# Performance work log

Hardware: AMD Instinct MI355X
Metric: run time of the kernel (lower is better)

## Reference

```python
import jax, jax.numpy as jnp
import numpy as np

# Dimensions per init_kwargs
B, S, D = 2, 2048, 1024          # batch, seq, hidden_size
F = 4096                          # intermediate_size
E, K = 8, 2                       # moe_num_experts, moe_top_k
EPS = 1e-9


def setup_inputs() -> dict:
    key = jax.random.key(0)
    k1, k2, k3, k4 = jax.random.split(key, 4)
    x = jax.random.normal(k1, (B, S, D), dtype=jnp.float32)
    # gate: Linear(D, E, bias=False) -> stored as [D, E] for x @ w_gate
    w_gate = jax.random.normal(k2, (D, E), dtype=jnp.float32) * 0.02
    # per-expert gate_up_proj: Linear(D, 2F, bias=False), stacked over experts -> [E, D, 2F]
    w_gate_up = jax.random.normal(k3, (E, D, 2 * F), dtype=jnp.float32) * 0.02
    # per-expert down_proj: Linear(F, D, bias=False), stacked -> [E, F, D]
    w_down = jax.random.normal(k4, (E, F, D), dtype=jnp.float32) * 0.02
    return {"x": x, "w_gate": w_gate, "w_gate_up": w_gate_up, "w_down": w_down}


def reference(x, w_gate, w_gate_up, w_down):
    # Router
    gate_logits = x @ w_gate                       # [B,S,E]
    gate_probs = jax.nn.softmax(gate_logits, axis=-1)
    # top-k masking + renormalization (top_k < num_experts)
    topk_vals, topk_idx = jax.lax.top_k(gate_probs, K)           # [B,S,K]
    masked = jnp.sum(jax.nn.one_hot(topk_idx, E, dtype=gate_probs.dtype)
                     * topk_vals[..., None], axis=-2)            # [B,S,E]
    denom = jnp.maximum(jnp.sum(masked, axis=-1, keepdims=True), EPS)
    gate_probs = masked / denom

    # Dense per-expert SwiGLU FFN on all tokens (faithful to reference impl)
    gu = jnp.einsum('bsd,edh->ebsh', x, w_gate_up)               # [E,B,S,2F]
    g, u = jnp.split(gu, 2, axis=-1)                             # [E,B,S,F] each
    act = jax.nn.silu(g) * u                                     # [E,B,S,F]
    expert_out = jnp.einsum('ebsf,efd->ebsd', act, w_down)       # [E,B,S,D]

    # Gate-weighted combine
    return jnp.einsum('bse,ebsd->bsd', gate_probs, expert_out)   # [B,S,D]
```

## Files before the change

kernel.cpp:

```cpp
#include <hip/hip_runtime.h>
#include <stdint.h>

#define NTOK 4096
#define DMODEL 1024
#define FF 4096
#define NEXP 8

typedef __bf16 bf16x8 __attribute__((ext_vector_type(8)));
typedef float f32x4 __attribute__((ext_vector_type(4)));
typedef unsigned short u16x8 __attribute__((ext_vector_type(8)));

__device__ __forceinline__ unsigned short f2bf(float f) {
  union { float f; unsigned u; } v; v.f = f;
  unsigned r = v.u + 0x7fffu + ((v.u >> 16) & 1u);
  return (unsigned short)(r >> 16);
}

__global__ __launch_bounds__(256) void k_convert_x(const float4* __restrict__ in,
                                                   ushort4* __restrict__ out, int n4) {
  int stride = gridDim.x * blockDim.x;
  for (int i = blockIdx.x * blockDim.x + threadIdx.x; i < n4; i += stride) {
    float4 v = in[i];
    out[i] = make_ushort4(f2bf(v.x), f2bf(v.y), f2bf(v.z), f2bf(v.w));
  }
}

__global__ __launch_bounds__(256) void k_transpose_bf16(const float* __restrict__ in,
                                                        unsigned short* __restrict__ out,
                                                        int R, int C) {
  __shared__ float tile[64][65];
  const size_t slab = (size_t)R * C;
  const float* ip = in + slab * blockIdx.z;
  unsigned short* op = out + slab * blockIdx.z;
  int c0 = blockIdx.x * 64, r0 = blockIdx.y * 64;
  int tx = threadIdx.x & 15, ty = threadIdx.x >> 4;
#pragma unroll
  for (int i = 0; i < 4; ++i) {
    int r = ty + 16 * i;
    float4 v = *(const float4*)(ip + (size_t)(r0 + r) * C + c0 + tx * 4);
    tile[r][tx * 4 + 0] = v.x;
    tile[r][tx * 4 + 1] = v.y;
    tile[r][tx * 4 + 2] = v.z;
    tile[r][tx * 4 + 3] = v.w;
  }
  __syncthreads();
  int w = threadIdx.x >> 6, lane = threadIdx.x & 63;
  int rc = (lane & 7) * 8;
#pragma unroll
  for (int pass = 0; pass < 2; ++pass) {
    int c = pass * 32 + w * 8 + (lane >> 3);
    u16x8 o;
#pragma unroll
    for (int j = 0; j < 8; ++j) o[j] = f2bf(tile[rc + j][c]);
    *(u16x8*)(op + (size_t)(c0 + c) * R + r0 + rc) = o;
  }
}

__global__ __launch_bounds__(256) void k_router(const float* __restrict__ x,
                                                const float* __restrict__ wg,
                                                int* __restrict__ cnt,
                                                int* __restrict__ elist,
                                                float* __restrict__ gw) {
  int wave = threadIdx.x >> 6, lane = threadIdx.x & 63;
  int t = blockIdx.x * 4 + wave;
  const float* xp = x + (size_t)t * DMODEL;
  float a[8] = {0, 0, 0, 0, 0, 0, 0, 0};
#pragma unroll
  for (int i = 0; i < DMODEL / 64; ++i) {
    int d = lane + 64 * i;
    float xv = xp[d];
    float4 w0 = *(const float4*)(wg + d * 8);
    float4 w1 = *(const float4*)(wg + d * 8 + 4);
    a[0] += xv * w0.x; a[1] += xv * w0.y; a[2] += xv * w0.z; a[3] += xv * w0.w;
    a[4] += xv * w1.x; a[5] += xv * w1.y; a[6] += xv * w1.z; a[7] += xv * w1.w;
  }
#pragma unroll
  for (int off = 32; off > 0; off >>= 1)
#pragma unroll
    for (int e = 0; e < 8; ++e) a[e] += __shfl_down(a[e], off, 64);
  if (lane == 0) {
    int e0 = 0;
    for (int e = 1; e < 8; ++e) if (a[e] > a[e0]) e0 = e;
    int e1 = (e0 == 0) ? 1 : 0;
    for (int e = 0; e < 8; ++e) if (e != e0 && a[e] > a[e1]) e1 = e;
    float p = __expf(a[e1] - a[e0]);
    float inv = 1.0f / (1.0f + p);
    int p0 = atomicAdd(&cnt[e0], 1);
    elist[e0 * NTOK + p0] = 2 * t;
    gw[2 * t] = inv;
    int p1 = atomicAdd(&cnt[e1], 1);
    elist[e1 * NTOK + p1] = 2 * t + 1;
    gw[2 * t + 1] = p * inv;
  }
}

__global__ __launch_bounds__(512, 4) void k_gemm1(const unsigned short* __restrict__ xb,
                                                  const unsigned short* __restrict__ wgu,
                                                  const int* __restrict__ cnt,
                                                  const int* __restrict__ elist,
                                                  unsigned short* __restrict__ act)
{
  __shared__ __align__(16) unsigned short sA[2][128 * 64];
  __shared__ __align__(16) unsigned short sB[2][128 * 64];

  const int e = blockIdx.z;
  const int n_e = cnt[e];
  const int m0 = blockIdx.y * 128;
  if (m0 >= n_e) return;
  const int c0 = blockIdx.x * 64;
  int abase = 0;
#pragma unroll
  for (int j = 0; j < NEXP; ++j) abase += (j < e) ? cnt[j] : 0;
  const int tid = threadIdx.x;
  const int w = tid >> 6, lane = tid & 63;
  const int wr = w >> 2, wc = w & 3;
  const int* el = elist + e * NTOK;
  const int csub = ((lane & 7) ^ (lane >> 3)) * 8;
  const int srow = w * 8 + (lane >> 3);

  int tokrow[2];
  size_t baddr[2];
  const unsigned short* wb = wgu + (size_t)e * (2 * FF) * DMODEL;
#pragma unroll
  for (int i = 0; i < 2; ++i) {
    int r = i * 64 + srow;
    int idx = m0 + r;
    tokrow[i] = el[idx < n_e ? idx : 0] >> 1;
    int strip = r >> 5, off = r & 31;
    int wrow = (off < 16) ? (c0 + strip * 16 + off) : (FF + c0 + strip * 16 + off - 16);
    baddr[i] = (size_t)wrow * DMODEL;
  }

  f32x4 acc[4][2];
  f32x4 zero = {0.f, 0.f, 0.f, 0.f};
#pragma unroll
  for (int m = 0; m < 4; ++m)
#pragma unroll
    for (int n = 0; n < 2; ++n) acc[m][n] = zero;

  auto stage = [&](int buf, int k0) {
#pragma unroll
    for (int i = 0; i < 2; ++i) {
      const unsigned short* g2 = xb + (size_t)tokrow[i] * DMODEL + k0 + csub;
      __builtin_amdgcn_global_load_lds((const __attribute__((address_space(1))) void*)g2,
                                       (__attribute__((address_space(3))) void*)(&sA[buf][(i * 64 + w * 8) * 64]),
                                       16, 0, 0);
    }
#pragma unroll
    for (int i = 0; i < 2; ++i) {
      const unsigned short* g2 = wb + baddr[i] + k0 + csub;
      __builtin_amdgcn_global_load_lds((const __attribute__((address_space(1))) void*)g2,
                                       (__attribute__((address_space(3))) void*)(&sB[buf][(i * 64 + w * 8) * 64]),
                                       16, 0, 0);
    }
  };

  auto compute = [&](int buf) {
#pragma unroll
    for (int kk = 0; kk < 2; ++kk) {
      const int xk = ((kk * 4 + (lane >> 4)) ^ (lane & 7)) * 8;
      bf16x8 af[4], bf[2];
#pragma unroll
      for (int m = 0; m < 4; ++m)
        af[m] = *(const bf16x8*)(&sA[buf][(wr * 64 + m * 16 + (lane & 15)) * 64 + xk]);
#pragma unroll
      for (int n = 0; n < 2; ++n)
        bf[n] = *(const bf16x8*)(&sB[buf][(wc * 32 + n * 16 + (lane & 15)) * 64 + xk]);
#pragma unroll
      for (int m = 0; m < 4; ++m)
#pragma unroll
        for (int n = 0; n < 2; ++n)
          acc[m][n] = __builtin_amdgcn_mfma_f32_16x16x32_bf16(af[m], bf[n], acc[m][n], 0, 0, 0);
    }
  };

  stage(0, 0);
  __syncthreads();
  int cur = 0;
  for (int t = 0; t < DMODEL / 64; ++t) {
    if (t + 1 < DMODEL / 64) stage(cur ^ 1, (t + 1) * 64);
    compute(cur);
    __syncthreads();
    cur ^= 1;
  }

#pragma unroll
  for (int m = 0; m < 4; ++m) {
#pragma unroll
    for (int r = 0; r < 4; ++r) {
      int idx = m0 + wr * 64 + m * 16 + (lane >> 4) * 4 + r;
      if (idx < n_e) {
        unsigned short* ap = act + (size_t)(abase + idx) * FF + c0 + wc * 16;
        float gv = acc[m][0][r];
        float u = acc[m][1][r];
        float s = gv / (1.0f + __expf(-gv));
        ap[lane & 15] = f2bf(s * u);
      }
    }
  }
}

__global__ __launch_bounds__(256, 4) void k_gemm2(const unsigned short* __restrict__ actb,
                                                  const unsigned short* __restrict__ wd,
                                                  const int* __restrict__ cnt,
                                                  const int* __restrict__ elist,
                                                  const float* __restrict__ gw,
                                                  float* __restrict__ out)
{
  __shared__ __align__(16) unsigned short sA[128 * 64];
  __shared__ __align__(16) unsigned short sB[128 * 64];

  const int bid = blockIdx.x;
  const int e = bid & 7;
  const int within = bid >> 3;
  const int kc = within >> 8;
  const int y = (within >> 3) & 31;
  const int xcol = within & 7;
  const int n_e = cnt[e];
  const int m0 = y * 128;
  if (m0 >= n_e) return;
  const int n0 = xcol * 128;
  int abase = 0;
#pragma unroll
  for (int j = 0; j < NEXP; ++j) abase += (j < e) ? cnt[j] : 0;
  const int tid = threadIdx.x;
  const int w = tid >> 6, lane = tid & 63;
  const int wr = w >> 1, wc = w & 1;
  const int* el = elist + e * NTOK;
  const int csub = ((lane & 7) ^ (lane >> 3)) * 8;

  int arow[4];
  size_t baddr[4];
  const unsigned short* wb = wd + (size_t)e * DMODEL * FF;
#pragma unroll
  for (int i = 0; i < 4; ++i) {
    int r = i * 32 + w * 8 + (lane >> 3);
    int idx = m0 + r;
    arow[i] = abase + (idx < n_e ? idx : 0);
    baddr[i] = (size_t)(n0 + r) * FF;
  }

  f32x4 acc[4][4];
  f32x4 zero = {0.f, 0.f, 0.f, 0.f};
#pragma unroll
  for (int m = 0; m < 4; ++m)
#pragma unroll
    for (int n = 0; n < 4; ++n) acc[m][n] = zero;

  const int kbeg = kc * 1024, kend = kbeg + 1024;
  for (int k0 = kbeg; k0 < kend; k0 += 64) {
#pragma unroll
    for (int i = 0; i < 4; ++i) {
      const unsigned short* g2 = actb + (size_t)arow[i] * FF + k0 + csub;
      __builtin_amdgcn_global_load_lds((const __attribute__((address_space(1))) void*)g2,
                                       (__attribute__((address_space(3))) void*)(&sA[(i * 32 + w * 8) * 64]),
                                       16, 0, 0);
    }
#pragma unroll
    for (int i = 0; i < 4; ++i) {
      const unsigned short* g2 = wb + baddr[i] + k0 + csub;
      __builtin_amdgcn_global_load_lds((const __attribute__((address_space(1))) void*)g2,
                                       (__attribute__((address_space(3))) void*)(&sB[(i * 32 + w * 8) * 64]),
                                       16, 0, 0);
    }
    __syncthreads();
#pragma unroll
    for (int kk = 0; kk < 2; ++kk) {
      const int xk = ((kk * 4 + (lane >> 4)) ^ (lane & 7)) * 8;
      bf16x8 af[4], bf[4];
#pragma unroll
      for (int m = 0; m < 4; ++m)
        af[m] = *(const bf16x8*)(&sA[(wr * 64 + m * 16 + (lane & 15)) * 64 + xk]);
#pragma unroll
      for (int n = 0; n < 4; ++n)
        bf[n] = *(const bf16x8*)(&sB[(wc * 64 + n * 16 + (lane & 15)) * 64 + xk]);
#pragma unroll
      for (int m = 0; m < 4; ++m)
#pragma unroll
        for (int n = 0; n < 4; ++n)
          acc[m][n] = __builtin_amdgcn_mfma_f32_16x16x32_bf16(af[m], bf[n], acc[m][n], 0, 0, 0);
    }
    __syncthreads();
  }

#pragma unroll
  for (int m = 0; m < 4; ++m) {
#pragma unroll
    for (int r = 0; r < 4; ++r) {
      int idx = m0 + wr * 64 + m * 16 + (lane >> 4) * 4 + r;
      if (idx < n_e) {
        int p = el[idx];
        float wgt = gw[p];
        float* op = out + (size_t)(p >> 1) * DMODEL + n0 + wc * 64;
#pragma unroll
        for (int n = 0; n < 4; ++n)
          atomicAdd(&op[n * 16 + (lane & 15)], acc[m][n][r] * wgt);
      }
    }
  }
}

extern "C" void kernel_launch(void* const* d_in, const int* in_sizes, int n_in,
                              void* d_out, int out_size, void* d_ws, size_t ws_size,
                              hipStream_t stream) {
  const float* x   = (const float*)d_in[0];
  const float* wg  = (const float*)d_in[1];
  const float* wgu = (const float*)d_in[2];
  const float* wd  = (const float*)d_in[3];
  float* out = (float*)d_out;

  char* ws = (char*)d_ws;
  size_t off = 0;
  auto alloc = [&](size_t bytes) -> char* {
    char* p = ws + off;
    off += (bytes + 255) & ~(size_t)255;
    return p;
  };
  unsigned short* wgu_t = (unsigned short*)alloc((size_t)NEXP * 2 * FF * DMODEL * 2);
  unsigned short* wd_t  = (unsigned short*)alloc((size_t)NEXP * DMODEL * FF * 2);
  unsigned short* actb  = (unsigned short*)alloc((size_t)2 * NTOK * FF * 2);
  unsigned short* xb    = (unsigned short*)alloc((size_t)NTOK * DMODEL * 2);
  int* elist            = (int*)alloc((size_t)NEXP * NTOK * 4);
  float* gw             = (float*)alloc((size_t)2 * NTOK * 4);
  int* cnt              = (int*)alloc(256);
  if (off > ws_size) return;

  hipMemsetAsync(cnt, 0, 256, stream);
  hipMemsetAsync(out, 0, (size_t)NTOK * DMODEL * 4, stream);
  k_convert_x<<<1024, 256, 0, stream>>>((const float4*)x, (ushort4*)xb, NTOK * DMODEL / 4);
  k_transpose_bf16<<<dim3(2 * FF / 64, DMODEL / 64, NEXP), 256, 0, stream>>>(wgu, wgu_t, DMODEL, 2 * FF);
  k_transpose_bf16<<<dim3(DMODEL / 64, FF / 64, NEXP), 256, 0, stream>>>(wd, wd_t, FF, DMODEL);
  k_router<<<NTOK / 4, 256, 0, stream>>>(x, wg, cnt, elist, gw);
  k_gemm1<<<dim3(FF / 64, NTOK / 128, NEXP), 512, 0, stream>>>(xb, wgu_t, cnt, elist, actb);
  k_gemm2<<<8192, 256, 0, stream>>>(actb, wd_t, cnt, elist, gw, out);
}
```

Measured before the change: 582.2 us.

## Double-buffer gemm2 LDS tiles and remove split-K atomics

Rewrites the down-projection GEMM to process the full K dimension per block instead of four split-K chunks, and double-buffers the A/B LDS tiles so the next tile's global-to-LDS loads overlap the current MFMA work. Blocks grow to 512 threads with each wave computing a 64x32 sub-tile. This cuts the atomic adds to the output by a factor of four and hides load latency, but reduces the number of blocks and doubles LDS usage, which may lower occupancy and parallelism.

```diff
diff --git a/kernel.cpp b/kernel.cpp
--- a/kernel.cpp
+++ b/kernel.cpp
@@ -200,21 +200,20 @@
   }
 }
 
-__global__ __launch_bounds__(256, 4) void k_gemm2(const unsigned short* __restrict__ actb,
+__global__ __launch_bounds__(512, 4) void k_gemm2(const unsigned short* __restrict__ actb,
                                                   const unsigned short* __restrict__ wd,
                                                   const int* __restrict__ cnt,
                                                   const int* __restrict__ elist,
                                                   const float* __restrict__ gw,
                                                   float* __restrict__ out)
 {
-  __shared__ __align__(16) unsigned short sA[128 * 64];
-  __shared__ __align__(16) unsigned short sB[128 * 64];
+  __shared__ __align__(16) unsigned short sA[2][128 * 64];
+  __shared__ __align__(16) unsigned short sB[2][128 * 64];
 
   const int bid = blockIdx.x;
   const int e = bid & 7;
   const int within = bid >> 3;
-  const int kc = within >> 8;
-  const int y = (within >> 3) & 31;
+  const int y = within >> 3;
   const int xcol = within & 7;
   const int n_e = cnt[e];
   const int m0 = y * 128;
@@ -225,62 +224,72 @@
   for (int j = 0; j < NEXP; ++j) abase += (j < e) ? cnt[j] : 0;
   const int tid = threadIdx.x;
   const int w = tid >> 6, lane = tid & 63;
-  const int wr = w >> 1, wc = w & 1;
+  const int wr = w >> 2, wc = w & 3;
   const int* el = elist + e * NTOK;
   const int csub = ((lane & 7) ^ (lane >> 3)) * 8;
-
-  int arow[4];
-  size_t baddr[4];
+  const int srow = w * 8 + (lane >> 3);
+
+  int arow[2];
+  size_t baddr[2];
   const unsigned short* wb = wd + (size_t)e * DMODEL * FF;
 #pragma unroll
-  for (int i = 0; i < 4; ++i) {
-    int r = i * 32 + w * 8 + (lane >> 3);
-    int idx = m0 + r;
+  for (int i = 0; i < 2; ++i) {
+    int idx = m0 + i * 64 + srow;
     arow[i] = abase + (idx < n_e ? idx : 0);
-    baddr[i] = (size_t)(n0 + r) * FF;
-  }
-
-  f32x4 acc[4][4];
+    baddr[i] = (size_t)(n0 + i * 64 + srow) * FF;
+  }
+
+  f32x4 acc[4][2];
   f32x4 zero = {0.f, 0.f, 0.f, 0.f};
 #pragma unroll
   for (int m = 0; m < 4; ++m)
 #pragma unroll
-    for (int n = 0; n < 4; ++n) acc[m][n] = zero;
-
-  const int kbeg = kc * 1024, kend = kbeg + 1024;
-  for (int k0 = kbeg; k0 < kend; k0 += 64) {
-#pragma unroll
-    for (int i = 0; i < 4; ++i) {
+    for (int n = 0; n < 2; ++n) acc[m][n] = zero;
+
+  auto stage = [&](int buf, int k0) {
+#pragma unroll
+    for (int i = 0; i < 2; ++i) {
       const unsigned short* g2 = actb + (size_t)arow[i] * FF + k0 + csub;
       __builtin_amdgcn_global_load_lds((const __attribute__((address_space(1))) void*)g2,
-                                       (__attribute__((address_space(3))) void*)(&sA[(i * 32 + w * 8) * 64]),
+                                       (__attribute__((address_space(3))) void*)(&sA[buf][(i * 64 + w * 8) * 64]),
                                        16, 0, 0);
     }
 #pragma unroll
-    for (int i = 0; i < 4; ++i) {
+    for (int i = 0; i < 2; ++i) {
       const unsigned short* g2 = wb + baddr[i] + k0 + csub;
       __builtin_amdgcn_global_load_lds((const __attribute__((address_space(1))) void*)g2,
-                                       (__attribute__((address_space(3))) void*)(&sB[(i * 32 + w * 8) * 64]),
+                                       (__attribute__((address_space(3))) void*)(&sB[buf][(i * 64 + w * 8) * 64]),
                                        16, 0, 0);
     }
-    __syncthreads();
+  };
+
+  auto compute = [&](int buf) {
 #pragma unroll
     for (int kk = 0; kk < 2; ++kk) {
       const int xk = ((kk * 4 + (lane >> 4)) ^ (lane & 7)) * 8;
-      bf16x8 af[4], bf[4];
+      bf16x8 af[4], bf[2];
 #pragma unroll
       for (int m = 0; m < 4; ++m)
-        af[m] = *(const bf16x8*)(&sA[(wr * 64 + m * 16 + (lane & 15)) * 64 + xk]);
-#pragma unroll
-      for (int n = 0; n < 4; ++n)
-        bf[n] = *(const bf16x8*)(&sB[(wc * 64 + n * 16 + (lane & 15)) * 64 + xk]);
+        af[m] = *(const bf16x8*)(&sA[buf][(wr * 64 + m * 16 + (lane & 15)) * 64 + xk]);
+#pragma unroll
+      for (int n = 0; n < 2; ++n)
+        bf[n] = *(const bf16x8*)(&sB[buf][(wc * 32 + n * 16 + (lane & 15)) * 64 + xk]);
 #pragma unroll
       for (int m = 0; m < 4; ++m)
 #pragma unroll
-        for (int n = 0; n < 4; ++n)
+        for (int n = 0; n < 2; ++n)
           acc[m][n] = __builtin_amdgcn_mfma_f32_16x16x32_bf16(af[m], bf[n], acc[m][n], 0, 0, 0);
     }
+  };
+
+  stage(0, 0);
+  __syncthreads();
+  int cur = 0;
+  for (int t = 0; t < FF / 64; ++t) {
+    if (t + 1 < FF / 64) stage(cur ^ 1, (t + 1) * 64);
+    compute(cur);
     __syncthreads();
+    cur ^= 1;
   }
 
 #pragma unroll
@@ -291,9 +300,9 @@
       if (idx < n_e) {
         int p = el[idx];
         float wgt = gw[p];
-        float* op = out + (size_t)(p >> 1) * DMODEL + n0 + wc * 64;
-#pragma unroll
-        for (int n = 0; n < 4; ++n)
+        float* op = out + (size_t)(p >> 1) * DMODEL + n0 + wc * 32;
+#pragma unroll
+        for (int n = 0; n < 2; ++n)
           atomicAdd(&op[n * 16 + (lane & 15)], acc[m][n][r] * wgt);
       }
     }
@@ -332,5 +341,5 @@
   k_transpose_bf16<<<dim3(DMODEL / 64, FF / 64, NEXP), 256, 0, stream>>>(wd, wd_t, FF, DMODEL);
   k_router<<<NTOK / 4, 256, 0, stream>>>(x, wg, cnt, elist, gw);
   k_gemm1<<<dim3(FF / 64, NTOK / 128, NEXP), 512, 0, stream>>>(xb, wgu_t, cnt, elist, actb);
-  k_gemm2<<<8192, 256, 0, stream>>>(actb, wd_t, cnt, elist, gw, out);
-}
+  k_gemm2<<<2048, 512, 0, stream>>>(actb, wd_t, cnt, elist, gw, out);
+}
```

New measurement: 588.0 us. No clear change (+1.0%).

## Replace split-K atomics in down-proj with per-slot stores and combine kernel

Applied to the files above, without the earlier changes.

The down-projection GEMM no longer splits K four ways with float atomicAdd into the output. Each block now runs the full FF reduction and writes a weighted result to a per-(token, slot) buffer, and a new combine kernel sums the two slots per token. Activations are stored indexed by slot id instead of by a compacted expert offset, and the block-to-tile mapping is changed. This removes atomic traffic and the output memset, at the cost of an extra 32MB buffer pass, 4x fewer gemm2 blocks (lower parallelism) and scattered activation rows.

```diff
diff --git a/kernel.cpp b/kernel.cpp
--- a/kernel.cpp
+++ b/kernel.cpp
@@ -108,9 +108,6 @@
   const int m0 = blockIdx.y * 128;
   if (m0 >= n_e) return;
   const int c0 = blockIdx.x * 64;
-  int abase = 0;
-#pragma unroll
-  for (int j = 0; j < NEXP; ++j) abase += (j < e) ? cnt[j] : 0;
   const int tid = threadIdx.x;
   const int w = tid >> 6, lane = tid & 63;
   const int wr = w >> 2, wc = w & 3;
@@ -190,7 +187,8 @@
     for (int r = 0; r < 4; ++r) {
       int idx = m0 + wr * 64 + m * 16 + (lane >> 4) * 4 + r;
       if (idx < n_e) {
-        unsigned short* ap = act + (size_t)(abase + idx) * FF + c0 + wc * 16;
+        int p = el[idx];
+        unsigned short* ap = act + (size_t)p * FF + c0 + wc * 16;
         float gv = acc[m][0][r];
         float u = acc[m][1][r];
         float s = gv / (1.0f + __expf(-gv));
@@ -205,38 +203,34 @@
                                                   const int* __restrict__ cnt,
                                                   const int* __restrict__ elist,
                                                   const float* __restrict__ gw,
-                                                  float* __restrict__ out)
+                                                  float* __restrict__ out_slot)
 {
   __shared__ __align__(16) unsigned short sA[128 * 64];
   __shared__ __align__(16) unsigned short sB[128 * 64];
 
   const int bid = blockIdx.x;
-  const int e = bid & 7;
-  const int within = bid >> 3;
-  const int kc = within >> 8;
-  const int y = (within >> 3) & 31;
-  const int xcol = within & 7;
+  const int orig = (bid & 7) * 256 + (bid >> 3);
+  const int g = orig >> 5;
+  const int y = orig & 31;
+  const int e = g >> 3;
   const int n_e = cnt[e];
   const int m0 = y * 128;
   if (m0 >= n_e) return;
-  const int n0 = xcol * 128;
-  int abase = 0;
-#pragma unroll
-  for (int j = 0; j < NEXP; ++j) abase += (j < e) ? cnt[j] : 0;
+  const int n0 = (g & 7) * 128;
   const int tid = threadIdx.x;
   const int w = tid >> 6, lane = tid & 63;
   const int wr = w >> 1, wc = w & 1;
   const int* el = elist + e * NTOK;
   const int csub = ((lane & 7) ^ (lane >> 3)) * 8;
 
-  int arow[4];
+  int prow[4];
   size_t baddr[4];
   const unsigned short* wb = wd + (size_t)e * DMODEL * FF;
 #pragma unroll
   for (int i = 0; i < 4; ++i) {
     int r = i * 32 + w * 8 + (lane >> 3);
     int idx = m0 + r;
-    arow[i] = abase + (idx < n_e ? idx : 0);
+    prow[i] = el[idx < n_e ? idx : 0];
     baddr[i] = (size_t)(n0 + r) * FF;
   }
 
@@ -247,11 +241,10 @@
 #pragma unroll
     for (int n = 0; n < 4; ++n) acc[m][n] = zero;
 
-  const int kbeg = kc * 1024, kend = kbeg + 1024;
-  for (int k0 = kbeg; k0 < kend; k0 += 64) {
+  for (int k0 = 0; k0 < FF; k0 += 64) {
 #pragma unroll
     for (int i = 0; i < 4; ++i) {
-      const unsigned short* g2 = actb + (size_t)arow[i] * FF + k0 + csub;
+      const unsigned short* g2 = actb + (size_t)prow[i] * FF + k0 + csub;
       __builtin_amdgcn_global_load_lds((const __attribute__((address_space(1))) void*)g2,
                                        (__attribute__((address_space(3))) void*)(&sA[(i * 32 + w * 8) * 64]),
                                        16, 0, 0);
@@ -291,12 +284,26 @@
       if (idx < n_e) {
         int p = el[idx];
         float wgt = gw[p];
-        float* op = out + (size_t)(p >> 1) * DMODEL + n0 + wc * 64;
+        float* op = out_slot + (size_t)p * DMODEL + n0 + wc * 64;
 #pragma unroll
         for (int n = 0; n < 4; ++n)
-          atomicAdd(&op[n * 16 + (lane & 15)], acc[m][n][r] * wgt);
+          op[n * 16 + (lane & 15)] = acc[m][n][r] * wgt;
       }
     }
+  }
+}
+
+__global__ __launch_bounds__(256) void k_combine(const float4* __restrict__ slot,
+                                                 float4* __restrict__ out, int n4) {
+  int stride = gridDim.x * blockDim.x;
+  for (int i = blockIdx.x * blockDim.x + threadIdx.x; i < n4; i += stride) {
+    int t = i >> 8;
+    int j = i & 255;
+    float4 a = slot[(size_t)(2 * t) * 256 + j];
+    float4 b = slot[(size_t)(2 * t + 1) * 256 + j];
+    float4 o;
+    o.x = a.x + b.x; o.y = a.y + b.y; o.z = a.z + b.z; o.w = a.w + b.w;
+    out[i] = o;
   }
 }
 
@@ -319,6 +326,7 @@
   unsigned short* wgu_t = (unsigned short*)alloc((size_t)NEXP * 2 * FF * DMODEL * 2);
   unsigned short* wd_t  = (unsigned short*)alloc((size_t)NEXP * DMODEL * FF * 2);
   unsigned short* actb  = (unsigned short*)alloc((size_t)2 * NTOK * FF * 2);
+  float* out_slot       = (float*)alloc((size_t)2 * NTOK * DMODEL * 4);
   unsigned short* xb    = (unsigned short*)alloc((size_t)NTOK * DMODEL * 2);
   int* elist            = (int*)alloc((size_t)NEXP * NTOK * 4);
   float* gw             = (float*)alloc((size_t)2 * NTOK * 4);
@@ -326,11 +334,11 @@
   if (off > ws_size) return;
 
   hipMemsetAsync(cnt, 0, 256, stream);
-  hipMemsetAsync(out, 0, (size_t)NTOK * DMODEL * 4, stream);
   k_convert_x<<<1024, 256, 0, stream>>>((const float4*)x, (ushort4*)xb, NTOK * DMODEL / 4);
   k_transpose_bf16<<<dim3(2 * FF / 64, DMODEL / 64, NEXP), 256, 0, stream>>>(wgu, wgu_t, DMODEL, 2 * FF);
   k_transpose_bf16<<<dim3(DMODEL / 64, FF / 64, NEXP), 256, 0, stream>>>(wd, wd_t, FF, DMODEL);
   k_router<<<NTOK / 4, 256, 0, stream>>>(x, wg, cnt, elist, gw);
   k_gemm1<<<dim3(FF / 64, NTOK / 128, NEXP), 512, 0, stream>>>(xb, wgu_t, cnt, elist, actb);
-  k_gemm2<<<8192, 256, 0, stream>>>(actb, wd_t, cnt, elist, gw, out);
-}
+  k_gemm2<<<2048, 256, 0, stream>>>(actb, wd_t, cnt, elist, gw, out_slot);
+  k_combine<<<2048, 256, 0, stream>>>((const float4*)out_slot, (float4*)out, NTOK * DMODEL / 4);
+}
```

Result: no change. 575.0 us (-1.2%).
